# Kernel tuning notes

Hardware: AMD Instinct MI355X
Metric: run time of the kernel (lower is better)

Reference implementation:

```python
import jax, jax.numpy as jnp
import numpy as np

B, C, H, W = 8, 256, 64, 64
CELLS_PER_IMAGE = 16
N = B * CELLS_PER_IMAGE  # total cells


def setup_inputs() -> dict:
    key = jax.random.key(0)
    k1, k2 = jax.random.split(key)
    feature_maps = jax.random.normal(k1, (B, C, H, W), dtype=jnp.float32)
    # dense-ish boolean cell masks; with 4096 pixels per mask every cell is nonempty
    cell_masks = jax.random.bernoulli(k2, p=0.25, shape=(N, H, W))
    cell_counts = jnp.full((B,), CELLS_PER_IMAGE, dtype=jnp.int32)
    return {"feature_maps": feature_maps, "cell_masks": cell_masks, "cell_counts": cell_counts}


def reference(feature_maps, cell_masks, cell_counts):
    # method='max', positions=False (constructor defaults).
    # Map each cell to its source image: repeat(arange(B), counts) with a
    # static total length so it is jit-compatible.
    n_cells = cell_masks.shape[0]
    batch = feature_maps.shape[0]
    cell_batch = jnp.repeat(jnp.arange(batch), cell_counts, total_repeat_length=n_cells)
    x = feature_maps[cell_batch]  # (N, C, H, W) gathered per cell
    neg_inf = jnp.asarray(-jnp.inf, x.dtype)
    masked = jnp.where(cell_masks[:, None, :, :], x, neg_inf)
    # max over the masked pixels of each cell -> (N, C)
    return jnp.max(masked, axis=(2, 3))
```

## Files before the change

kernel.cpp:

```cpp
#include <hip/hip_runtime.h>
#include <hip/hip_bf16.h>


#define HW    4096
#define BIMG  8
#define CCH   256
#define NCELL 128
#define CG    4

__device__ __forceinline__ void cell_range(const int* counts, int b, int& start, int& cnt) {
    start = 0;
    for (int i = 0; i < b; ++i) start += counts[i];
    if (start > NCELL) start = NCELL;
    cnt = counts[b];
    if (b == BIMG - 1 && start + cnt < NCELL) cnt = NCELL - start;
    if (cnt > 16) cnt = 16;
    if (start + cnt > NCELL) cnt = NCELL - start;
    if (cnt < 0) cnt = 0;
}

__global__ __launch_bounds__(256)
void roipool_fused(const void* __restrict__ featv,
                   const void* __restrict__ maskv,
                   const int* __restrict__ counts,
                   void* __restrict__ outv) {
    const int b   = blockIdx.y;
    const int cg0 = blockIdx.x * CG;
    const int tid = threadIdx.x;
    const float NEG = -__builtin_inff();
    const unsigned NEGI = 0xFF800000u;

    __shared__ int s_msize;
    __shared__ int s_fbf16;

    if (tid < 64) {
        const unsigned* mw = (const unsigned*)maskv;
        unsigned ow = mw[tid * 4] | mw[tid * 4 + 1] | mw[tid * 4 + 2] | mw[tid * 4 + 3];
        #pragma unroll
        for (int d = 32; d >= 1; d >>= 1) ow |= __shfl_down(ow, d, 64);
        const unsigned* fw_ = (const unsigned*)featv;
        unsigned w = fw_[tid];
        unsigned eb = (w >> 8) & 0x7F;
        int hit = (eb >= 0x3B && eb <= 0x41);
        unsigned long long bm = __ballot(hit);
        if (tid == 0) {
            unsigned or0 = ow & 0xFFu, or1 = (ow >> 8) & 0xFFu;
            int s;
            if (or1 == 0)                         s = 4;
            else if (or0 == 0x80 || or0 == 0x00)  s = 2;
            else                                  s = 1;
            s_msize = s;
            s_fbf16 = (__popcll(bm) >= 48);
        }
    }
    __syncthreads();
    const int msize = s_msize;
    const int fbf16 = s_fbf16;

    int start, cnt;
    cell_range(counts, b, start, cnt);

    unsigned pm[16];
    #pragma unroll
    for (int i = 0; i < 16; ++i) pm[i] = 0;
    const int p0 = tid * 16;
    const unsigned char* mb = (const unsigned char*)maskv;

    if (msize == 1) {
        for (int j = 0; j < cnt; ++j) {
            uint4 mv = *(const uint4*)(mb + ((size_t)(start + j) << 12) + p0);
            unsigned wd[4] = {mv.x, mv.y, mv.z, mv.w};
            #pragma unroll
            for (int i = 0; i < 16; ++i) {
                unsigned byte = (wd[i >> 2] >> ((i & 3) * 8)) & 0xFFu;
                pm[i] |= (byte ? 1u : 0u) << j;
            }
        }
    } else if (msize == 2) {
        for (int j = 0; j < cnt; ++j) {
            const unsigned char* base = mb + (((size_t)(start + j) << 12) + p0) * 2;
            uint4 a  = *(const uint4*)(base);
            uint4 c2 = *(const uint4*)(base + 16);
            unsigned wd[8] = {a.x, a.y, a.z, a.w, c2.x, c2.y, c2.z, c2.w};
            #pragma unroll
            for (int i = 0; i < 16; ++i) {
                unsigned h = (wd[i >> 1] >> ((i & 1) * 16)) & 0xFFFFu;
                pm[i] |= (h ? 1u : 0u) << j;
            }
        }
    } else {
        for (int j = 0; j < cnt; ++j) {
            const unsigned char* base = mb + (((size_t)(start + j) << 12) + p0) * 4;
            #pragma unroll
            for (int q = 0; q < 4; ++q) {
                uint4 a = *(const uint4*)(base + q * 16);
                unsigned wd[4] = {a.x, a.y, a.z, a.w};
                #pragma unroll
                for (int r = 0; r < 4; ++r)
                    pm[q * 4 + r] |= (wd[r] ? 1u : 0u) << j;
            }
        }
    }

    __shared__ float red[256 * 17];
    __shared__ float red2[16 * 17];

    for (int cc = 0; cc < CG; ++cc) {
        const int c = cg0 + cc;
        unsigned pe[8], po[8];
        if (fbf16) {
            const unsigned short* fp = (const unsigned short*)featv
                                     + (((size_t)(b * CCH + c)) << 12) + p0;
            uint4 f0 = *(const uint4*)(fp);
            uint4 f1 = *(const uint4*)(fp + 8);
            unsigned w8[8] = {f0.x, f0.y, f0.z, f0.w, f1.x, f1.y, f1.z, f1.w};
            #pragma unroll
            for (int k = 0; k < 8; ++k) {
                pe[k] = w8[k] << 16;
                po[k] = w8[k] & 0xFFFF0000u;
            }
        } else {
            const float* fp = (const float*)featv + (((size_t)(b * CCH + c)) << 12) + p0;
            #pragma unroll
            for (int q = 0; q < 4; ++q) {
                uint4 a = *(const uint4*)(fp + q * 4);
                unsigned w4[4] = {a.x, a.y, a.z, a.w};
                pe[q * 2]     = w4[0]; po[q * 2]     = w4[1];
                pe[q * 2 + 1] = w4[2]; po[q * 2 + 1] = w4[3];
            }
        }

        float vmax[16];
        #pragma unroll
        for (int j = 0; j < 16; ++j) vmax[j] = NEG;

        #pragma unroll
        for (int k = 0; k < 8; ++k) {
            const unsigned fe = pe[k], fo = po[k];
            const unsigned me = pm[2 * k];
            const unsigned mo = pm[2 * k + 1];
            #pragma unroll
            for (int j = 0; j < 16; ++j) {
                unsigned m0 = (unsigned)(((int)(me << (31 - j))) >> 31);
                unsigned m1 = (unsigned)(((int)(mo << (31 - j))) >> 31);
                float s0 = __uint_as_float((fe & m0) | (NEGI & ~m0));
                float s1 = __uint_as_float((fo & m1) | (NEGI & ~m1));
                vmax[j] = fmaxf(fmaxf(vmax[j], s0), s1);
            }
        }

        #pragma unroll
        for (int j = 0; j < 16; ++j) red[tid * 17 + j] = vmax[j];
        __syncthreads();
        {
            const int jj = tid & 15;
            const int g  = tid >> 4;
            float m = NEG;
            #pragma unroll
            for (int r = 0; r < 16; ++r)
                m = fmaxf(m, red[(g * 16 + r) * 17 + jj]);
            red2[g * 17 + jj] = m;
        }
        __syncthreads();
        if (tid < 16) {
            float m2 = NEG;
            #pragma unroll
            for (int g2 = 0; g2 < 16; ++g2)
                m2 = fmaxf(m2, red2[g2 * 17 + tid]);
            if (tid < cnt) {
                size_t oi = (size_t)(start + tid) * CCH + c;
                if (fbf16) ((__hip_bfloat16*)outv)[oi] = __float2bfloat16(m2);
                else       ((float*)outv)[oi] = m2;
            }
        }
        __syncthreads();
    }
}

extern "C" void kernel_launch(void* const* d_in, const int* in_sizes, int n_in,
                              void* d_out, int out_size, void* d_ws, size_t ws_size,
                              hipStream_t stream) {
    const void* feat  = d_in[0];
    const void* masks = d_in[1];
    const int* counts = (const int*)d_in[2];

    dim3 grid(CCH / CG, BIMG);
    roipool_fused<<<grid, 256, 0, stream>>>(feat, masks, counts, d_out);
}
```

Baseline: 107.9 us.

## Pre-pack cell masks into per-pixel bitmasks in a separate kernel

Splits the fused kernel in two. A first kernel packs each image's 16 cell masks into one 16-bit word per pixel in workspace. The main kernel then processes one channel per block instead of four, loading the packed mask words rather than re-reading and packing raw masks in every block. This removes the redundant mask reads across the 64 channel-group blocks per image, at the cost of an extra launch, a workspace round trip, and more blocks each doing a shorter reduction.

```diff
diff --git a/kernel.cpp b/kernel.cpp
--- a/kernel.cpp
+++ b/kernel.cpp
@@ -6,7 +6,6 @@
 #define BIMG  8
 #define CCH   256
 #define NCELL 128
-#define CG    4
 
 __device__ __forceinline__ void cell_range(const int* counts, int b, int& start, int& cnt) {
     start = 0;
@@ -20,29 +19,20 @@
 }
 
 __global__ __launch_bounds__(256)
-void roipool_fused(const void* __restrict__ featv,
-                   const void* __restrict__ maskv,
-                   const int* __restrict__ counts,
-                   void* __restrict__ outv) {
-    const int b   = blockIdx.y;
-    const int cg0 = blockIdx.x * CG;
+void pack_masks(const void* __restrict__ maskv,
+                const int* __restrict__ counts,
+                unsigned short* __restrict__ packed) {
+    const int idx = blockIdx.x * blockDim.x + threadIdx.x;
     const int tid = threadIdx.x;
-    const float NEG = -__builtin_inff();
-    const unsigned NEGI = 0xFF800000u;
+    const int b = idx >> 12;
+    const int p = idx & (HW - 1);
 
     __shared__ int s_msize;
-    __shared__ int s_fbf16;
-
     if (tid < 64) {
         const unsigned* mw = (const unsigned*)maskv;
         unsigned ow = mw[tid * 4] | mw[tid * 4 + 1] | mw[tid * 4 + 2] | mw[tid * 4 + 3];
         #pragma unroll
         for (int d = 32; d >= 1; d >>= 1) ow |= __shfl_down(ow, d, 64);
-        const unsigned* fw_ = (const unsigned*)featv;
-        unsigned w = fw_[tid];
-        unsigned eb = (w >> 8) & 0x7F;
-        int hit = (eb >= 0x3B && eb <= 0x41);
-        unsigned long long bm = __ballot(hit);
         if (tid == 0) {
             unsigned or0 = ow & 0xFFu, or1 = (ow >> 8) & 0xFFu;
             int s;
@@ -50,130 +40,127 @@
             else if (or0 == 0x80 || or0 == 0x00)  s = 2;
             else                                  s = 1;
             s_msize = s;
-            s_fbf16 = (__popcll(bm) >= 48);
         }
     }
     __syncthreads();
     const int msize = s_msize;
+
+    int start, cnt;
+    cell_range(counts, b, start, cnt);
+
+    unsigned w = 0;
+    if (msize == 2) {
+        const unsigned short* mh = (const unsigned short*)maskv;
+        for (int j = 0; j < cnt; ++j)
+            w |= (mh[(size_t)(start + j) * HW + p] ? 1u : 0u) << j;
+    } else if (msize == 4) {
+        const unsigned* mw = (const unsigned*)maskv;
+        for (int j = 0; j < cnt; ++j)
+            w |= (mw[(size_t)(start + j) * HW + p] ? 1u : 0u) << j;
+    } else {
+        const unsigned char* mb = (const unsigned char*)maskv;
+        for (int j = 0; j < cnt; ++j)
+            w |= (mb[(size_t)(start + j) * HW + p] ? 1u : 0u) << j;
+    }
+    packed[idx] = (unsigned short)w;
+}
+
+__global__ __launch_bounds__(256, 4)
+void roipool_main(const void* __restrict__ featv,
+                  const unsigned short* __restrict__ packed,
+                  const int* __restrict__ counts,
+                  void* __restrict__ outv) {
+    const int c   = blockIdx.x;
+    const int b   = blockIdx.y;
+    const int tid = threadIdx.x;
+    const float NEG = -__builtin_inff();
+    const unsigned NEGI = 0xFF800000u;
+
+    __shared__ int s_fbf16;
+    if (tid < 64) {
+        const unsigned* fw_ = (const unsigned*)featv;
+        unsigned w = fw_[tid];
+        unsigned eb = (w >> 8) & 0x7F;
+        unsigned long long bm = __ballot(eb >= 0x3B && eb <= 0x41);
+        if (tid == 0) s_fbf16 = (__popcll(bm) >= 48);
+    }
+    __syncthreads();
     const int fbf16 = s_fbf16;
 
     int start, cnt;
     cell_range(counts, b, start, cnt);
 
-    unsigned pm[16];
-    #pragma unroll
-    for (int i = 0; i < 16; ++i) pm[i] = 0;
     const int p0 = tid * 16;
-    const unsigned char* mb = (const unsigned char*)maskv;
 
-    if (msize == 1) {
-        for (int j = 0; j < cnt; ++j) {
-            uint4 mv = *(const uint4*)(mb + ((size_t)(start + j) << 12) + p0);
-            unsigned wd[4] = {mv.x, mv.y, mv.z, mv.w};
-            #pragma unroll
-            for (int i = 0; i < 16; ++i) {
-                unsigned byte = (wd[i >> 2] >> ((i & 3) * 8)) & 0xFFu;
-                pm[i] |= (byte ? 1u : 0u) << j;
-            }
-        }
-    } else if (msize == 2) {
-        for (int j = 0; j < cnt; ++j) {
-            const unsigned char* base = mb + (((size_t)(start + j) << 12) + p0) * 2;
-            uint4 a  = *(const uint4*)(base);
-            uint4 c2 = *(const uint4*)(base + 16);
-            unsigned wd[8] = {a.x, a.y, a.z, a.w, c2.x, c2.y, c2.z, c2.w};
-            #pragma unroll
-            for (int i = 0; i < 16; ++i) {
-                unsigned h = (wd[i >> 1] >> ((i & 1) * 16)) & 0xFFFFu;
-                pm[i] |= (h ? 1u : 0u) << j;
-            }
+    uint4 pa = *(const uint4*)(packed + ((size_t)b << 12) + p0);
+    uint4 pb = *(const uint4*)(packed + ((size_t)b << 12) + p0 + 8);
+    unsigned pmw[8] = {pa.x, pa.y, pa.z, pa.w, pb.x, pb.y, pb.z, pb.w};
+
+    unsigned pe[8], po[8];
+    if (fbf16) {
+        const unsigned short* fp = (const unsigned short*)featv
+                                 + (((size_t)(b * CCH + c)) << 12) + p0;
+        uint4 f0 = *(const uint4*)(fp);
+        uint4 f1 = *(const uint4*)(fp + 8);
+        unsigned w8[8] = {f0.x, f0.y, f0.z, f0.w, f1.x, f1.y, f1.z, f1.w};
+        #pragma unroll
+        for (int k = 0; k < 8; ++k) {
+            pe[k] = w8[k] << 16;
+            po[k] = w8[k] & 0xFFFF0000u;
         }
     } else {
-        for (int j = 0; j < cnt; ++j) {
-            const unsigned char* base = mb + (((size_t)(start + j) << 12) + p0) * 4;
-            #pragma unroll
-            for (int q = 0; q < 4; ++q) {
-                uint4 a = *(const uint4*)(base + q * 16);
-                unsigned wd[4] = {a.x, a.y, a.z, a.w};
-                #pragma unroll
-                for (int r = 0; r < 4; ++r)
-                    pm[q * 4 + r] |= (wd[r] ? 1u : 0u) << j;
-            }
+        const float* fp = (const float*)featv + (((size_t)(b * CCH + c)) << 12) + p0;
+        #pragma unroll
+        for (int q = 0; q < 4; ++q) {
+            uint4 a = *(const uint4*)(fp + q * 4);
+            pe[q * 2]     = a.x; po[q * 2]     = a.y;
+            pe[q * 2 + 1] = a.z; po[q * 2 + 1] = a.w;
+        }
+    }
+
+    float vmax[16];
+    #pragma unroll
+    for (int j = 0; j < 16; ++j) vmax[j] = NEG;
+
+    #pragma unroll
+    for (int k = 0; k < 8; ++k) {
+        const unsigned fe = pe[k], fo = po[k];
+        const unsigned mw = pmw[k];
+        #pragma unroll
+        for (int j = 0; j < 16; ++j) {
+            unsigned m0 = (unsigned)(((int)(mw << (31 - j))) >> 31);
+            unsigned m1 = (unsigned)(((int)(mw << (15 - j))) >> 31);
+            float s0 = __uint_as_float((fe & m0) | (NEGI & ~m0));
+            float s1 = __uint_as_float((fo & m1) | (NEGI & ~m1));
+            vmax[j] = fmaxf(fmaxf(vmax[j], s0), s1);
         }
     }
 
     __shared__ float red[256 * 17];
     __shared__ float red2[16 * 17];
-
-    for (int cc = 0; cc < CG; ++cc) {
-        const int c = cg0 + cc;
-        unsigned pe[8], po[8];
-        if (fbf16) {
-            const unsigned short* fp = (const unsigned short*)featv
-                                     + (((size_t)(b * CCH + c)) << 12) + p0;
-            uint4 f0 = *(const uint4*)(fp);
-            uint4 f1 = *(const uint4*)(fp + 8);
-            unsigned w8[8] = {f0.x, f0.y, f0.z, f0.w, f1.x, f1.y, f1.z, f1.w};
-            #pragma unroll
-            for (int k = 0; k < 8; ++k) {
-                pe[k] = w8[k] << 16;
-                po[k] = w8[k] & 0xFFFF0000u;
-            }
-        } else {
-            const float* fp = (const float*)featv + (((size_t)(b * CCH + c)) << 12) + p0;
-            #pragma unroll
-            for (int q = 0; q < 4; ++q) {
-                uint4 a = *(const uint4*)(fp + q * 4);
-                unsigned w4[4] = {a.x, a.y, a.z, a.w};
-                pe[q * 2]     = w4[0]; po[q * 2]     = w4[1];
-                pe[q * 2 + 1] = w4[2]; po[q * 2 + 1] = w4[3];
-            }
+    #pragma unroll
+    for (int j = 0; j < 16; ++j) red[tid * 17 + j] = vmax[j];
+    __syncthreads();
+    {
+        const int jj = tid & 15;
+        const int g  = tid >> 4;
+        float m = NEG;
+        #pragma unroll
+        for (int r = 0; r < 16; ++r)
+            m = fmaxf(m, red[(g * 16 + r) * 17 + jj]);
+        red2[g * 17 + jj] = m;
+    }
+    __syncthreads();
+    if (tid < 16) {
+        float m2 = NEG;
+        #pragma unroll
+        for (int g2 = 0; g2 < 16; ++g2)
+            m2 = fmaxf(m2, red2[g2 * 17 + tid]);
+        if (tid < cnt) {
+            size_t oi = (size_t)(start + tid) * CCH + c;
+            if (fbf16) ((__hip_bfloat16*)outv)[oi] = __float2bfloat16(m2);
+            else       ((float*)outv)[oi] = m2;
         }
-
-        float vmax[16];
-        #pragma unroll
-        for (int j = 0; j < 16; ++j) vmax[j] = NEG;
-
-        #pragma unroll
-        for (int k = 0; k < 8; ++k) {
-            const unsigned fe = pe[k], fo = po[k];
-            const unsigned me = pm[2 * k];
-            const unsigned mo = pm[2 * k + 1];
-            #pragma unroll
-            for (int j = 0; j < 16; ++j) {
-                unsigned m0 = (unsigned)(((int)(me << (31 - j))) >> 31);
-                unsigned m1 = (unsigned)(((int)(mo << (31 - j))) >> 31);
-                float s0 = __uint_as_float((fe & m0) | (NEGI & ~m0));
-                float s1 = __uint_as_float((fo & m1) | (NEGI & ~m1));
-                vmax[j] = fmaxf(fmaxf(vmax[j], s0), s1);
-            }
-        }
-
-        #pragma unroll
-        for (int j = 0; j < 16; ++j) red[tid * 17 + j] = vmax[j];
-        __syncthreads();
-        {
-            const int jj = tid & 15;
-            const int g  = tid >> 4;
-            float m = NEG;
-            #pragma unroll
-            for (int r = 0; r < 16; ++r)
-                m = fmaxf(m, red[(g * 16 + r) * 17 + jj]);
-            red2[g * 17 + jj] = m;
-        }
-        __syncthreads();
-        if (tid < 16) {
-            float m2 = NEG;
-            #pragma unroll
-            for (int g2 = 0; g2 < 16; ++g2)
-                m2 = fmaxf(m2, red2[g2 * 17 + tid]);
-            if (tid < cnt) {
-                size_t oi = (size_t)(start + tid) * CCH + c;
-                if (fbf16) ((__hip_bfloat16*)outv)[oi] = __float2bfloat16(m2);
-                else       ((float*)outv)[oi] = m2;
-            }
-        }
-        __syncthreads();
     }
 }
 
@@ -183,7 +170,10 @@
     const void* feat  = d_in[0];
     const void* masks = d_in[1];
     const int* counts = (const int*)d_in[2];
+    unsigned short* packed = (unsigned short*)d_ws;
 
-    dim3 grid(CCH / CG, BIMG);
-    roipool_fused<<<grid, 256, 0, stream>>>(feat, masks, counts, d_out);
+    pack_masks<<<(BIMG * HW) / 256, 256, 0, stream>>>(masks, counts, packed);
+
+    dim3 grid(CCH, BIMG);
+    roipool_main<<<grid, 256, 0, stream>>>(feat, packed, counts, d_out);
 }
```

Measured after the change: 87.10 us. -19.3%, faster.
